# Kernel optimization log

Measured on AMD Instinct MI355X. Metric: run time of the kernel, lower is better.

Reference implementation:

```python
import jax, jax.numpy as jnp
import numpy as np
from jax import lax

FILTERS = 32
NEIGH = 5


def _conv3d_same(x, w, b=None):
    out = lax.conv_general_dilated(x, w, window_strides=(1, 1, 1), padding='SAME',
                                   dimension_numbers=('NCDHW', 'OIDHW', 'NCDHW'))
    return out if b is None else out + b[None, :, None, None, None]


def _avgpool2(x):
    s = lax.reduce_window(x, 0.0, lax.add, (1, 1, 2, 2, 2), (1, 1, 2, 2, 2), 'VALID')
    return s * 0.125


def _grid_sample_3d(vol, grid):
    # trilinear, zeros padding, align_corners=False (torch defaults)
    Din, Hin, Win = vol.shape
    ix = ((grid[..., 0] + 1.0) * Win - 1.0) * 0.5
    iy = ((grid[..., 1] + 1.0) * Hin - 1.0) * 0.5
    iz = ((grid[..., 2] + 1.0) * Din - 1.0) * 0.5
    x0f, y0f, z0f = jnp.floor(ix), jnp.floor(iy), jnp.floor(iz)
    wx, wy, wz = ix - x0f, iy - y0f, iz - z0f
    x0 = x0f.astype(jnp.int32); y0 = y0f.astype(jnp.int32); z0 = z0f.astype(jnp.int32)

    def tap(z, y, x, w):
        valid = (z >= 0) & (z < Din) & (y >= 0) & (y < Hin) & (x >= 0) & (x < Win)
        v = vol[jnp.clip(z, 0, Din - 1), jnp.clip(y, 0, Hin - 1), jnp.clip(x, 0, Win - 1)]
        return jnp.where(valid, v, 0.0) * w

    return (tap(z0,     y0,     x0,     (1 - wz) * (1 - wy) * (1 - wx))
          + tap(z0,     y0,     x0 + 1, (1 - wz) * (1 - wy) * wx)
          + tap(z0,     y0 + 1, x0,     (1 - wz) * wy * (1 - wx))
          + tap(z0,     y0 + 1, x0 + 1, (1 - wz) * wy * wx)
          + tap(z0 + 1, y0,     x0,     wz * (1 - wy) * (1 - wx))
          + tap(z0 + 1, y0,     x0 + 1, wz * (1 - wy) * wx)
          + tap(z0 + 1, y0 + 1, x0,     wz * wy * (1 - wx))
          + tap(z0 + 1, y0 + 1, x0 + 1, wz * wy * wx))


def _forward(x, conv_w, conv_b, gaus_w):
    D = _avgpool2(_conv3d_same(x, conv_w, conv_b))           # (B, c, h, w, d)
    p = _conv3d_same(D, gaus_w)                              # (B, c, h, w, d)
    B, c, h, w, d = D.shape
    # normalized coordinate field P: (3, h, w, d)
    P = jnp.stack([
        jnp.broadcast_to(jnp.arange(h, dtype=D.dtype)[:, None, None] / (h - 1), (h, w, d)),
        jnp.broadcast_to(jnp.arange(w, dtype=D.dtype)[None, :, None] / (w - 1), (h, w, d)),
        jnp.broadcast_to(jnp.arange(d, dtype=D.dtype)[None, None, :] / (d - 1), (h, w, d)),
    ])
    # (B, 3, c, h, w, d) -> (3B, c, h, w, d) for a single batched gaussian conv
    D_mul = (P[None, :, None] * D[:, None]).reshape(3 * B, c, h, w, d)
    allf = _conv3d_same(D_mul, gaus_w).reshape(B, 3, c, h, w, d)
    filt = jnp.clip(allf / (p[:, None] + 1e-6) * 2.0 - 1.0, -1.0, 1.0)
    grids = jnp.transpose(filt, (0, 2, 3, 4, 5, 1))          # (B, c, h, w, d, 3)
    Bx, Cx, Hx, Wx, Dx = x.shape
    vols = x.reshape(B * c, Hx, Wx, Dx)
    g = grids.reshape(B * c, h, w, d, 3)
    y = jax.vmap(_grid_sample_3d)(vols, g).reshape(B, c, h, w, d)
    return y, D, jnp.mean(grids, axis=1)


def setup_inputs() -> dict:
    key = jax.random.key(0)
    k1, k2, k3 = jax.random.split(key, 3)
    x = jax.random.normal(k1, (2, FILTERS, 64, 64, 64), dtype=jnp.float32)
    fan_in = FILTERS * 3 * 3 * 3
    conv_w = (jax.random.normal(k2, (FILTERS, FILTERS, 3, 3, 3), dtype=jnp.float32)
              / np.float32(np.sqrt(fan_in)))
    conv_b = jax.random.normal(k3, (FILTERS,), dtype=jnp.float32) * 0.01
    # fixed gaussian kernel, replicated across in/out channels (as in makegaussian)
    center = NEIGH // 2
    co = np.arange(NEIGH) - center
    zz, yy, xx = np.meshgrid(co, co, co, indexing='ij')
    gk = np.exp(-4.0 * np.log(2.0) * (zz ** 2 + yy ** 2 + xx ** 2) / NEIGH ** 2).astype(np.float32)
    gaus_w = jnp.asarray(np.broadcast_to(gk, (FILTERS, FILTERS, NEIGH, NEIGH, NEIGH)).copy())
    return {"x": x, "conv_w": conv_w, "conv_b": conv_b, "gaus_w": gaus_w}


def reference(x, conv_w, conv_b, gaus_w):
    return _forward(x, conv_w, conv_b, gaus_w)
```

## Files before the change

### kernel.cpp

```cpp
#include <hip/hip_runtime.h>
#include <hip/hip_bf16.h>


#define XN 64
#define DN 32
#define C  32
#define XVOL (XN * XN * XN)
#define DVOL (DN * DN * DN)

typedef __attribute__((ext_vector_type(8))) short short8v;
typedef __attribute__((ext_vector_type(4))) float float4v;

struct __attribute__((packed, aligned(4))) f4u { float4v v; };
struct __attribute__((packed, aligned(4))) s8u { short8v v; };

static __device__ __forceinline__ short f2bf(float f) {
    union { float f; unsigned u; } v; v.f = f;
    unsigned r = (v.u + 0x7fffu + ((v.u >> 16) & 1u)) >> 16;
    return (short)r;
}

static __device__ __forceinline__ unsigned pk2(float a, float b) {
    __hip_bfloat162 h = __float22bfloat162_rn(float2{a, b});
    union { __hip_bfloat162 h2; unsigned u; } cv; cv.h2 = h;
    return cv.u;
}

static __device__ __forceinline__ float w4val(const float* __restrict__ conv_w,
                                              int ic, int u, int oc) {
    int uz = u >> 4, uy = (u >> 2) & 3, ux = u & 3;
    float s = 0.f;
    #pragma unroll
    for (int sz = 0; sz < 2; ++sz) {
        int tz = uz - sz; if (tz < 0 || tz > 2) continue;
        #pragma unroll
        for (int sy = 0; sy < 2; ++sy) {
            int ty = uy - sy; if (ty < 0 || ty > 2) continue;
            #pragma unroll
            for (int sx = 0; sx < 2; ++sx) {
                int tx = ux - sx; if (tx < 0 || tx > 2) continue;
                s += conv_w[(oc * C + ic) * 27 + tz * 9 + ty * 3 + tx];
            }
        }
    }
    return 0.125f * s;
}

__global__ __launch_bounds__(256) void k_prep(const float* __restrict__ conv_w,
                                              const float* __restrict__ conv_b,
                                              unsigned short* __restrict__ wfrag,
                                              float* __restrict__ wsum) {
    int bid = blockIdx.x;
    int tid = threadIdx.x;
    if (bid < 256) {
        int i = bid * 256 + tid;
        int e = i & 7;
        int l = (i >> 3) & 63;
        int sf = i >> 9;
        int f = sf & 1, step = sf >> 1;
        int oc = f * 16 + (l & 15);
        int k = step * 32 + ((l >> 4) * 8 + e);
        float v = w4val(conv_w, k >> 6, k & 63, oc);
        wfrag[i] = (unsigned short)f2bf(v);
        if (i == 0) {
            float s = 0.f;
            for (int o = 0; o < C; ++o) s += conv_b[o];
            wsum[2048] = s;
        }
    } else {
        int i2 = (bid - 256) * 256 + tid;
        int oc = tid & 31;
        int kk = i2 >> 5;
        float v = w4val(conv_w, kk >> 6, kk & 63, oc);
        v += __shfl_xor(v, 1, 64);
        v += __shfl_xor(v, 2, 64);
        v += __shfl_xor(v, 4, 64);
        v += __shfl_xor(v, 8, 64);
        v += __shfl_xor(v, 16, 64);
        if (oc == 0) wsum[kk] = v;
    }
}

#define NSTG (6 * 6 * 34)
#define TILEF (6 * 6 * 36)

__global__ __launch_bounds__(256) void k_conv_mfma(
        const float* __restrict__ x, const unsigned short* __restrict__ wfrag,
        const float* __restrict__ wsum, const float* __restrict__ bias,
        float* __restrict__ Dout, float* __restrict__ Dsum) {
    __shared__ float wsl[2112];
    __shared__ char wbuf[2 * 8320];
    __shared__ float tile[2][TILEF];
    int tid = threadIdx.x;
    for (int i = tid; i < 513; i += 256)
        *(float4v*)&wsl[i * 4] = *(const float4v*)&wsum[i * 4];

    int bid = blockIdx.x;
    int wid = (bid & 7) * 128 + (bid >> 3);
    int xt = wid & 1;
    int yt = (wid >> 1) & 15;
    int zt = (wid >> 5) & 15;
    int b  = wid >> 9;
    int w = tid >> 6, lane = tid & 63;
    int col = lane & 15, g = lane >> 4;
    int wpz = w >> 1, wpy = w & 1;
    int pz = zt * 2 + wpz, py = yt * 2 + wpy, px = xt * 16 + col;

    const float* xb = x + (size_t)b * C * XVOL;
    const char* wfb = (const char*)wfrag;
    int wsdst = (tid >> 6) * 1040 + (tid & 63) * 16;

    int gz0 = zt * 4 - 1, gy0 = yt * 4 - 1, gx0 = xt * 32 - 1;
    int  soff[5], sdst[5];
    bool sval[5], swr[5];
    #pragma unroll
    for (int it = 0; it < 5; ++it) {
        int i = tid + it * 256;
        int lx = i % 34; int r = i / 34; int ly = r % 6; int lz = r / 6;
        int gz = gz0 + lz, gy = gy0 + ly, gx = gx0 + lx;
        bool inr = i < NSTG;
        swr[it]  = inr;
        sval[it] = inr && (unsigned)gz < XN && (unsigned)gy < XN && (unsigned)gx < XN;
        soff[it] = ((gz & 63) * XN + (gy & 63)) * XN + (gx & 63);
        sdst[it] = inr ? (lz * 6 + ly) * 36 + lx : 0;
    }

    int base_g = ((2 * wpz + (g >> 1)) * 6 + 2 * wpy + (g & 1) * 2) * 36 + 2 * col;

    float4v acc0 = {0.f, 0.f, 0.f, 0.f};
    float4v acc1 = {0.f, 0.f, 0.f, 0.f};
    float4v dpv = {0.f, 0.f, 0.f, 0.f};
    float svA[5], svB[5];
    short8v sg0, sg1;

#define TLOAD(SV, j) do {                                                    \
    const float* xp = xb + (size_t)(j) * XVOL;                               \
    _Pragma("unroll")                                                        \
    for (int it = 0; it < 5; ++it)                                           \
        SV[it] = sval[it] ? xp[soff[it]] : 0.f;                              \
} while (0)

#define TWRITE(dst, SV) do {                                                 \
    _Pragma("unroll")                                                        \
    for (int it = 0; it < 5; ++it)                                           \
        if (swr[it]) (dst)[sdst[it]] = SV[it];                               \
} while (0)

#define WLOAD(st) do {                                                       \
    const char* wp = wfb + (size_t)(st) * 8192 + tid * 16;                   \
    sg0 = ((const s8u*)(wp))->v;                                             \
    sg1 = ((const s8u*)(wp + 4096))->v;                                      \
} while (0)

#define WWRITE(bf) do {                                                      \
    *(short8v*)(wbuf + (bf) * 8320 + wsdst) = sg0;                           \
    *(short8v*)(wbuf + (bf) * 8320 + 4160 + wsdst) = sg1;                    \
} while (0)

#define COMPT(ic) do {                                                       \
    const float* t = tile[(ic) & 1];                                         \
    _Pragma("unroll")                                                        \
    for (int h5 = 0; h5 < 2; ++h5) {                                         \
        int off0 = base_g + h5 * 432;                                        \
        float2 v01 = *(const float2*)&t[off0];                               \
        float2 v23 = *(const float2*)&t[off0 + 2];                           \
        float2 v45 = *(const float2*)&t[off0 + 36];                          \
        float2 v67 = *(const float2*)&t[off0 + 38];                          \
        float4v r0 = {v01.x, v01.y, v23.x, v23.y};                           \
        float4v r1 = {v45.x, v45.y, v67.x, v67.y};                           \
        const float4v wlo = *(const float4v*)&wsl[((ic) * 2 + h5) * 32 + g * 8];     \
        const float4v whi = *(const float4v*)&wsl[((ic) * 2 + h5) * 32 + g * 8 + 4]; \
        dpv += wlo * r0;                                                     \
        dpv += whi * r1;                                                     \
        union { short8v s; unsigned u[4]; } Bv;                              \
        Bv.u[0] = pk2(r0[0], r0[1]); Bv.u[1] = pk2(r0[2], r0[3]);            \
        Bv.u[2] = pk2(r1[0], r1[1]); Bv.u[3] = pk2(r1[2], r1[3]);            \
        const char* wl = wbuf + (((ic) >> 1) & 1) * 8320 + ((ic) & 1) * 4160 \
                         + lane * 16;                                        \
        short8v w0 = *(const short8v*)(wl + (h5 * 2) * 1040);                \
        short8v w1 = *(const short8v*)(wl + (h5 * 2 + 1) * 1040);            \
        acc0 = __builtin_amdgcn_mfma_f32_16x16x32_bf16(w0, Bv.s, acc0, 0, 0, 0); \
        acc1 = __builtin_amdgcn_mfma_f32_16x16x32_bf16(w1, Bv.s, acc1, 0, 0, 0); \
    }                                                                        \
} while (0)

    WLOAD(0);
    WWRITE(0);
    {
        float sv[5];
        TLOAD(sv, 0);
        TWRITE(tile[0], sv);
    }
    TLOAD(svB, 1);
    __syncthreads();

    for (int st = 0; st < 16; ++st) {
        int ic0 = 2 * st, ic1 = 2 * st + 1;
        if (st > 0) __syncthreads();
        TWRITE(tile[1], svB);
        if (ic0 + 2 < C) TLOAD(svA, ic0 + 2);
        if (st < 15) WLOAD(st + 1);
        COMPT(ic0);
        __syncthreads();
        if (ic0 + 2 < C) TWRITE(tile[0], svA);
        if (ic1 + 2 < C) TLOAD(svB, ic1 + 2);
        COMPT(ic1);
        if (st < 15) WWRITE((st + 1) & 1);
    }

#undef TLOAD
#undef TWRITE
#undef WLOAD
#undef WWRITE
#undef COMPT

    float dp = (dpv[0] + dpv[1]) + (dpv[2] + dpv[3]);
    dp += __shfl_xor(dp, 16, 64);
    dp += __shfl_xor(dp, 32, 64);

    int sp = pz * (DN * DN) + py * DN + px;
    float4v b0 = *(const float4v*)&bias[g * 4];
    float4v b1 = *(const float4v*)&bias[16 + g * 4];
    #pragma unroll
    for (int r = 0; r < 4; ++r) {
        int oc0 = g * 4 + r;
        int oc1 = 16 + g * 4 + r;
        Dout[(size_t)(b * C + oc0) * DVOL + sp] = acc0[r] + b0[r];
        Dout[(size_t)(b * C + oc1) * DVOL + sp] = acc1[r] + b1[r];
    }
    if (g == 0)
        Dsum[b * DVOL + sp] = dp + wsl[2048];
}

__global__ __launch_bounds__(256) void k_gauss(const float* __restrict__ Dsum,
                                               const float* __restrict__ gaus_w,
                                               float* __restrict__ filt,
                                               float* __restrict__ outg) {
    __shared__ float tg[8 * 12 * 12];
    __shared__ float gk[125];
    int bid = blockIdx.x;
    int xt = bid & 3, yt = (bid >> 2) & 3, zt = (bid >> 4) & 7, b = bid >> 7;
    int tid = threadIdx.x;
    if (tid < 125) gk[tid] = gaus_w[tid];
    const float* Ds = Dsum + b * DVOL;
    for (int i = tid; i < 1152; i += 256) {
        int lx = i % 12; int r = i / 12; int ly = r % 12; int lz = r / 12;
        int gz = zt * 4 - 2 + lz, gy = yt * 8 - 2 + ly, gx = xt * 8 - 2 + lx;
        float v = 0.f;
        if ((unsigned)gz < DN && (unsigned)gy < DN && (unsigned)gx < DN)
            v = Ds[(gz * DN + gy) * DN + gx];
        tg[i] = v;
    }
    __syncthreads();
    int px = tid & 7, py = (tid >> 3) & 7, pz = tid >> 6;
    const float inv31 = 1.f / 31.f;
    float zb = (float)(zt * 4 + pz - 2);
    float yb = (float)(yt * 8 + py - 2);
    float xb = (float)(xt * 8 + px - 2);
    float p = 0.f, a0 = 0.f, a1 = 0.f, a2 = 0.f;
    for (int tz = 0; tz < 5; ++tz)
    for (int ty = 0; ty < 5; ++ty) {
        int base = ((pz + tz) * 12 + py + ty) * 12 + px;
        #pragma unroll
        for (int tx = 0; tx < 5; ++tx) {
            float g = gk[tz * 25 + ty * 5 + tx];
            float v = g * tg[base + tx];
            p += v;
            a0 = fmaf(v, (zb + (float)tz) * inv31, a0);
            a1 = fmaf(v, (yb + (float)ty) * inv31, a1);
            a2 = fmaf(v, (xb + (float)tx) * inv31, a2);
        }
    }
    float denom = p + 1e-6f;
    float f0 = fminf(fmaxf(a0 / denom * 2.f - 1.f, -1.f), 1.f);
    float f1 = fminf(fmaxf(a1 / denom * 2.f - 1.f, -1.f), 1.f);
    float f2 = fminf(fmaxf(a2 / denom * 2.f - 1.f, -1.f), 1.f);
    int sp = ((zt * 4 + pz) * DN + yt * 8 + py) * DN + xt * 8 + px;
    filt[(b * 3 + 0) * DVOL + sp] = f0;
    filt[(b * 3 + 1) * DVOL + sp] = f1;
    filt[(b * 3 + 2) * DVOL + sp] = f2;
    outg[(size_t)(b * DVOL + sp) * 3 + 0] = f0;
    outg[(size_t)(b * DVOL + sp) * 3 + 1] = f1;
    outg[(size_t)(b * DVOL + sp) * 3 + 2] = f2;
}

__global__ __launch_bounds__(128) void k_sample(const float* __restrict__ x,
                                                const float* __restrict__ filt,
                                                float* __restrict__ y) {
    int bid = blockIdx.x;
    int wid = (bid & 7) * 1024 + (bid >> 3);
    int xt = wid & 1;
    int yt = (wid >> 1) & 7;
    int zt = (wid >> 4) & 15;
    int cgrp = (wid >> 8) & 15;
    int b  = wid >> 12;
    int tid = threadIdx.x;
    int px = tid & 15, py = (tid >> 4) & 3, pz = tid >> 6;
    int sp = ((zt * 2 + pz) * DN + yt * 4 + py) * DN + xt * 16 + px;
    const float* fb = filt + b * 3 * DVOL;
    float g0 = fb[sp], g1 = fb[DVOL + sp], g2 = fb[2 * DVOL + sp];

    float ix = ((g0 + 1.0f) * (float)XN - 1.0f) * 0.5f;
    float iy = ((g1 + 1.0f) * (float)XN - 1.0f) * 0.5f;
    float iz = ((g2 + 1.0f) * (float)XN - 1.0f) * 0.5f;
    float x0f = floorf(ix), y0f = floorf(iy), z0f = floorf(iz);
    float wx = ix - x0f, wyf = iy - y0f, wz = iz - z0f;
    int x0 = (int)x0f, y0i = (int)y0f, z0 = (int)z0f;

    int offs[8];
    float wts[8];
    #pragma unroll
    for (int t = 0; t < 8; ++t) {
        int dz = t >> 2, dy = (t >> 1) & 1, dx = t & 1;
        int zc = z0 + dz, yc = y0i + dy, xc = x0 + dx;
        bool valid = (unsigned)zc < (unsigned)XN && (unsigned)yc < (unsigned)XN &&
                     (unsigned)xc < (unsigned)XN;
        int zcl = min(max(zc, 0), XN - 1);
        int ycl = min(max(yc, 0), XN - 1);
        int xcl = min(max(xc, 0), XN - 1);
        offs[t] = zcl * (XN * XN) + ycl * XN + xcl;
        float w = (dz ? wz : 1.f - wz) * (dy ? wyf : 1.f - wyf) * (dx ? wx : 1.f - wx);
        wts[t] = valid ? w : 0.f;
    }

    const float* xc0 = x + (size_t)(b * C + cgrp * 2) * XVOL;
    float t0[8], t1[8];
    #pragma unroll
    for (int k = 0; k < 8; ++k) t0[k] = xc0[offs[k]];
    #pragma unroll
    for (int k = 0; k < 8; ++k) t1[k] = xc0[XVOL + offs[k]];

    float a0 = 0.f, a1 = 0.f;
    #pragma unroll
    for (int k = 0; k < 8; ++k) a0 = fmaf(wts[k], t0[k], a0);
    #pragma unroll
    for (int k = 0; k < 8; ++k) a1 = fmaf(wts[k], t1[k], a1);
    y[(size_t)(b * C + cgrp * 2 + 0) * DVOL + sp] = a0;
    y[(size_t)(b * C + cgrp * 2 + 1) * DVOL + sp] = a1;
}

extern "C" void kernel_launch(void* const* d_in, const int* in_sizes, int n_in,
                              void* d_out, int out_size, void* d_ws, size_t ws_size,
                              hipStream_t stream) {
    const float* x      = (const float*)d_in[0];
    const float* conv_w = (const float*)d_in[1];
    const float* conv_b = (const float*)d_in[2];
    const float* gaus_w = (const float*)d_in[3];

    float* out = (float*)d_out;
    float* y_out = out;
    float* D_out = out + (size_t)2097152;
    float* g_out = out + (size_t)4194304;

    float* ws   = (float*)d_ws;
    float* Dsum = ws;
    float* filt = ws + 65536;
    float* wsum = ws + 262144;
    unsigned short* wfrag = (unsigned short*)(ws + 264256);

    k_prep<<<dim3(512), dim3(256), 0, stream>>>(conv_w, conv_b, wfrag, wsum);
    k_conv_mfma<<<dim3(1024), dim3(256), 0, stream>>>(x, wfrag, wsum, conv_b,
                                                      D_out, Dsum);
    k_gauss<<<dim3(256), dim3(256), 0, stream>>>(Dsum, gaus_w, filt, g_out);
    k_sample<<<dim3(8192), dim3(128), 0, stream>>>(x, filt, y_out);
    (void)in_sizes; (void)n_in; (void)out_size; (void)ws_size;
}
```

Baseline: 84.51 us.

## Pipeline conv input channels in pairs with one barrier per pair

Restructures the conv MFMA main loop so that each iteration stages two input channels, both tile slices and their weight fragments, into a double-buffered shared tile pair. This halves the number of __syncthreads per block. The weight-sum table is now streamed per pair through a small double buffer instead of being preloaded whole into LDS, which shrinks shared memory. In exchange, each thread holds twice as many prefetch registers, so register pressure and occupancy may change.

```diff
diff --git a/kernel.cpp b/kernel.cpp
--- a/kernel.cpp
+++ b/kernel.cpp
@@ -88,12 +88,10 @@
         const float* __restrict__ x, const unsigned short* __restrict__ wfrag,
         const float* __restrict__ wsum, const float* __restrict__ bias,
         float* __restrict__ Dout, float* __restrict__ Dsum) {
-    __shared__ float wsl[2112];
+    __shared__ float tilepair[2][2 * TILEF];
     __shared__ char wbuf[2 * 8320];
-    __shared__ float tile[2][TILEF];
+    __shared__ float wsb[2][132];
     int tid = threadIdx.x;
-    for (int i = tid; i < 513; i += 256)
-        *(float4v*)&wsl[i * 4] = *(const float4v*)&wsum[i * 4];
 
     int bid = blockIdx.x;
     int wid = (bid & 7) * 128 + (bid >> 3);
@@ -130,35 +128,47 @@
     float4v acc0 = {0.f, 0.f, 0.f, 0.f};
     float4v acc1 = {0.f, 0.f, 0.f, 0.f};
     float4v dpv = {0.f, 0.f, 0.f, 0.f};
-    float svA[5], svB[5];
+    float svA[10], svB[10];
     short8v sg0, sg1;
-
-#define TLOAD(SV, j) do {                                                    \
-    const float* xp = xb + (size_t)(j) * XVOL;                               \
+    float wv;
+
+#define TLOADP(SV, p) do {                                                   \
+    const float* xp0 = xb + (size_t)(2 * (p)) * XVOL;                        \
     _Pragma("unroll")                                                        \
     for (int it = 0; it < 5; ++it)                                           \
-        SV[it] = sval[it] ? xp[soff[it]] : 0.f;                              \
-} while (0)
-
-#define TWRITE(dst, SV) do {                                                 \
+        SV[it] = sval[it] ? xp0[soff[it]] : 0.f;                             \
+    const float* xp1 = xp0 + XVOL;                                           \
     _Pragma("unroll")                                                        \
     for (int it = 0; it < 5; ++it)                                           \
-        if (swr[it]) (dst)[sdst[it]] = SV[it];                               \
-} while (0)
-
-#define WLOAD(st) do {                                                       \
-    const char* wp = wfb + (size_t)(st) * 8192 + tid * 16;                   \
+        SV[5 + it] = sval[it] ? xp1[soff[it]] : 0.f;                         \
+} while (0)
+
+#define TWRITEP(bf, SV) do {                                                 \
+    float* d0 = tilepair[bf];                                                \
+    _Pragma("unroll")                                                        \
+    for (int it = 0; it < 5; ++it)                                           \
+        if (swr[it]) d0[sdst[it]] = SV[it];                                  \
+    float* d1 = tilepair[bf] + TILEF;                                        \
+    _Pragma("unroll")                                                        \
+    for (int it = 0; it < 5; ++it)                                           \
+        if (swr[it]) d1[sdst[it]] = SV[5 + it];                              \
+} while (0)
+
+#define WLOAD(p) do {                                                        \
+    const char* wp = wfb + (size_t)(p) * 8192 + tid * 16;                    \
     sg0 = ((const s8u*)(wp))->v;                                             \
     sg1 = ((const s8u*)(wp + 4096))->v;                                      \
+    wv = (tid < 128) ? wsum[(p) * 128 + tid] : 0.f;                          \
 } while (0)
 
 #define WWRITE(bf) do {                                                      \
     *(short8v*)(wbuf + (bf) * 8320 + wsdst) = sg0;                           \
     *(short8v*)(wbuf + (bf) * 8320 + 4160 + wsdst) = sg1;                    \
-} while (0)
-
-#define COMPT(ic) do {                                                       \
-    const float* t = tile[(ic) & 1];                                         \
+    if (tid < 128) wsb[bf][tid] = wv;                                        \
+} while (0)
+
+#define COMPT(bf, icL) do {                                                  \
+    const float* t = tilepair[bf] + (icL) * TILEF;                           \
     _Pragma("unroll")                                                        \
     for (int h5 = 0; h5 < 2; ++h5) {                                         \
         int off0 = base_g + h5 * 432;                                        \
@@ -168,15 +178,14 @@
         float2 v67 = *(const float2*)&t[off0 + 38];                          \
         float4v r0 = {v01.x, v01.y, v23.x, v23.y};                           \
         float4v r1 = {v45.x, v45.y, v67.x, v67.y};                           \
-        const float4v wlo = *(const float4v*)&wsl[((ic) * 2 + h5) * 32 + g * 8];     \
-        const float4v whi = *(const float4v*)&wsl[((ic) * 2 + h5) * 32 + g * 8 + 4]; \
+        const float4v wlo = *(const float4v*)&wsb[bf][((icL) * 2 + h5) * 32 + g * 8];     \
+        const float4v whi = *(const float4v*)&wsb[bf][((icL) * 2 + h5) * 32 + g * 8 + 4]; \
         dpv += wlo * r0;                                                     \
         dpv += whi * r1;                                                     \
         union { short8v s; unsigned u[4]; } Bv;                              \
         Bv.u[0] = pk2(r0[0], r0[1]); Bv.u[1] = pk2(r0[2], r0[3]);            \
         Bv.u[2] = pk2(r1[0], r1[1]); Bv.u[3] = pk2(r1[2], r1[3]);            \
-        const char* wl = wbuf + (((ic) >> 1) & 1) * 8320 + ((ic) & 1) * 4160 \
-                         + lane * 16;                                        \
+        const char* wl = wbuf + (bf) * 8320 + (icL) * 4160 + lane * 16;      \
         short8v w0 = *(const short8v*)(wl + (h5 * 2) * 1040);                \
         short8v w1 = *(const short8v*)(wl + (h5 * 2 + 1) * 1040);            \
         acc0 = __builtin_amdgcn_mfma_f32_16x16x32_bf16(w0, Bv.s, acc0, 0, 0, 0); \
@@ -186,30 +195,29 @@
 
     WLOAD(0);
     WWRITE(0);
-    {
-        float sv[5];
-        TLOAD(sv, 0);
-        TWRITE(tile[0], sv);
-    }
-    TLOAD(svB, 1);
+    TLOADP(svA, 0);
+    TWRITEP(0, svA);
+    TLOADP(svB, 1);
     __syncthreads();
 
-    for (int st = 0; st < 16; ++st) {
-        int ic0 = 2 * st, ic1 = 2 * st + 1;
-        if (st > 0) __syncthreads();
-        TWRITE(tile[1], svB);
-        if (ic0 + 2 < C) TLOAD(svA, ic0 + 2);
-        if (st < 15) WLOAD(st + 1);
-        COMPT(ic0);
-        __syncthreads();
-        if (ic0 + 2 < C) TWRITE(tile[0], svA);
-        if (ic1 + 2 < C) TLOAD(svB, ic1 + 2);
-        COMPT(ic1);
-        if (st < 15) WWRITE((st + 1) & 1);
-    }
-
-#undef TLOAD
-#undef TWRITE
+    #pragma unroll 2
+    for (int p = 0; p < 16; ++p) {
+        int buf = p & 1;
+        if (p + 2 < 16) {
+            if (buf == 0) TLOADP(svA, p + 2); else TLOADP(svB, p + 2);
+        }
+        if (p + 1 < 16) WLOAD(p + 1);
+        COMPT(buf, 0);
+        COMPT(buf, 1);
+        if (p + 1 < 16) {
+            if (buf == 0) TWRITEP(1, svB); else TWRITEP(0, svA);
+            WWRITE(buf ^ 1);
+            __syncthreads();
+        }
+    }
+
+#undef TLOADP
+#undef TWRITEP
 #undef WLOAD
 #undef WWRITE
 #undef COMPT
@@ -229,7 +237,7 @@
         Dout[(size_t)(b * C + oc1) * DVOL + sp] = acc1[r] + b1[r];
     }
     if (g == 0)
-        Dsum[b * DVOL + sp] = dp + wsl[2048];
+        Dsum[b * DVOL + sp] = dp + wsum[2048];
 }
 
 __global__ __launch_bounds__(256) void k_gauss(const float* __restrict__ Dsum,
```

After: 97.10 us. 1.15x slower.
